# Performance work log

Measured on AMD Instinct MI355X. Metric: run time of the kernel, lower is better.

The kernel has to match this reference:

```python
import jax, jax.numpy as jnp
import numpy as np

NUM_ITERATIONS = 3

def _squash(s):
    # Original squash reduces over the trailing singleton dim -> elementwise.
    sn = s * s
    return sn * s / ((1.0 + sn) * jnp.sqrt(sn))

def setup_inputs() -> dict:
    key = jax.random.key(0)
    k1, k2 = jax.random.split(key)
    x = jax.random.normal(k1, (128, 1152, 8), dtype=jnp.float32)
    W = jax.random.normal(k2, (1, 1152, 16, 16, 8), dtype=jnp.float32)
    return {"x": x, "W": W}

def reference(x, W):
    # x: [B, R, I]; W: [1, R, C, O, I]
    Wr = W[0]  # [R, C, O, I]
    # u_hat = W @ x broadcast over capsules: [B, R, C, O]
    u_hat = jnp.einsum('rcoi,bri->brco', Wr, x)
    R, C = Wr.shape[0], Wr.shape[1]
    b = jnp.zeros((R, C), dtype=x.dtype)  # routing logits (shared across batch)
    v = None
    for it in range(NUM_ITERATIONS):
        # legacy F.softmax on [1,R,C,1] -> dim=1 == routes axis
        c = jax.nn.softmax(b, axis=0)  # [R, C]
        s = jnp.einsum('rc,brco->bco', c, u_hat)  # [B, C, O]
        v = _squash(s)
        if it < NUM_ITERATIONS - 1:
            # agreement: <u_hat, v> averaged over batch
            a = jnp.einsum('brco,bco->brc', u_hat, v).mean(axis=0)  # [R, C]
            b = b + a
    return v  # [B, C, O] == v_j.squeeze(1).squeeze(-1)
```

## Files before the change

### kernel.cpp

```cpp
#include <hip/hip_runtime.h>
#include <math.h>

#define B_   128
#define R_   1152
#define RS_  64
#define RCH_ 18
#define NBINS 72

#define WS_SP   0
#define WS_V    2097152
#define WS_BLOG 2129920
#define WS_CTRL 2148352
#define WS_WT   2150912

__device__ __forceinline__ float squashf(float s) {
    return s * fabsf(s) / (1.0f + s * s);
}

__global__ __launch_bounds__(512) void wtrans_k(const float* __restrict__ W,
                                                float* __restrict__ wt,
                                                float* __restrict__ ctrl) {
    const int r = blockIdx.x;
    const int t = threadIdx.x;
    __shared__ float4 sh[520];
    const float4* __restrict__ W4 = (const float4*)W;
    float4* __restrict__ Wt4 = (float4*)wt;

    if (r == 0) {
        for (int u = t; u < 2560; u += 512) ctrl[u] = 0.0f;
    }

    sh[(t & 7) * 65 + (t >> 3)] = W4[r * 512 + t];
    __syncthreads();
    Wt4[r * 512 + t] = sh[(t >> 6) * 65 + (t & 63)];
}

template <bool FIRST>
__global__ __launch_bounds__(256) void gemm_s_k(const float* __restrict__ x,
                                                const float* __restrict__ wt,
                                                const float* __restrict__ blog,
                                                const float* __restrict__ colbins,
                                                float* __restrict__ sp) {
    const int bt  = blockIdx.x;
    const int rs  = blockIdx.y;
    const int t   = threadIdx.x;
    const int co4 = t & 63;
    const int b4  = t >> 6;
    const int c   = co4 >> 2;
    const int r0  = rs * RCH_;

    __shared__ float4 xl4[288];
    __shared__ float  cwl[RCH_ * 16];
    __shared__ float  colinv_sh[16];
    __shared__ float  psum[256];

    const float4* __restrict__ X4  = (const float4*)x;
    const float4* __restrict__ Wt4 = (const float4*)wt;

    #pragma unroll
    for (int k = 0; k < 2; ++k) {
        const int u = t + k * 256;
        if (u < 288) {
            const int bl = u / 36, rem = u % 36;
            xl4[u] = X4[((bt * 8 + bl) * R_ + r0) * 2 + rem];
        }
    }

    if (!FIRST) {
        const int cc = t & 15, jb = t >> 4;
        float s = 0.f;
        for (int j = jb; j < NBINS; j += 16) s += colbins[j * 16 + cc];
        psum[t] = s;
        __syncthreads();
        if (t < 16) {
            float tot = 0.f;
            #pragma unroll
            for (int k2 = 0; k2 < 16; ++k2) tot += psum[k2 * 16 + t];
            colinv_sh[t] = 1.0f / tot;
        }
        __syncthreads();
        for (int u2 = t; u2 < RCH_ * 16; u2 += 256) {
            const int rl = u2 >> 4, c2 = u2 & 15;
            cwl[u2] = __expf(blog[(r0 + rl) * 16 + c2]) * colinv_sh[c2];
        }
    }
    __syncthreads();

    float acc[2][4];
    #pragma unroll
    for (int j = 0; j < 2; ++j)
        #pragma unroll
        for (int q = 0; q < 4; ++q) acc[j][q] = 0.f;

    #pragma unroll 3
    for (int rr = 0; rr < RCH_; ++rr) {
        const float cwv = FIRST ? (1.0f / (float)R_) : cwl[rr * 16 + c];
        const float4* wp = Wt4 + ((size_t)(r0 + rr) << 9) + co4;
        const float4 w0 = wp[  0], w1 = wp[ 64], w2 = wp[128], w3 = wp[192];
        const float4 w4 = wp[256], w5 = wp[320], w6 = wp[384], w7 = wp[448];
        #pragma unroll
        for (int j = 0; j < 2; ++j) {
            const float4 xa = xl4[(b4 * 2 + j) * 36 + rr * 2];
            const float4 xb = xl4[(b4 * 2 + j) * 36 + rr * 2 + 1];
            const float d0 = w0.x*xa.x + w0.y*xa.y + w0.z*xa.z + w0.w*xa.w
                           + w1.x*xb.x + w1.y*xb.y + w1.z*xb.z + w1.w*xb.w;
            const float d1 = w2.x*xa.x + w2.y*xa.y + w2.z*xa.z + w2.w*xa.w
                           + w3.x*xb.x + w3.y*xb.y + w3.z*xb.z + w3.w*xb.w;
            const float d2 = w4.x*xa.x + w4.y*xa.y + w4.z*xa.z + w4.w*xa.w
                           + w5.x*xb.x + w5.y*xb.y + w5.z*xb.z + w5.w*xb.w;
            const float d3 = w6.x*xa.x + w6.y*xa.y + w6.z*xa.z + w6.w*xa.w
                           + w7.x*xb.x + w7.y*xb.y + w7.z*xb.z + w7.w*xb.w;
            acc[j][0] = fmaf(cwv, d0, acc[j][0]);
            acc[j][1] = fmaf(cwv, d1, acc[j][1]);
            acc[j][2] = fmaf(cwv, d2, acc[j][2]);
            acc[j][3] = fmaf(cwv, d3, acc[j][3]);
        }
    }

    float4* sp4 = (float4*)sp;
    #pragma unroll
    for (int j = 0; j < 2; ++j) {
        const int b = bt * 8 + b4 * 2 + j;
        float4 o4; o4.x = acc[j][0]; o4.y = acc[j][1]; o4.z = acc[j][2]; o4.w = acc[j][3];
        sp4[(rs * B_ + b) * 64 + co4] = o4;
    }
}

__global__ __launch_bounds__(512) void reduce_squash_k(const float* __restrict__ sp,
                                                       float* __restrict__ outv) {
    const int t   = threadIdx.x;
    const int li  = t & 127;
    const int kq  = t >> 7;
    const int idx = blockIdx.x * 128 + li;
    const float* p = sp + (size_t)kq * 16 * 32768 + idx;
    float a0 = 0.f, a1 = 0.f, a2 = 0.f, a3 = 0.f;
    #pragma unroll
    for (int k = 0; k < 16; k += 4) {
        a0 += p[(k + 0) * 32768];
        a1 += p[(k + 1) * 32768];
        a2 += p[(k + 2) * 32768];
        a3 += p[(k + 3) * 32768];
    }
    __shared__ float red[512];
    red[t] = (a0 + a1) + (a2 + a3);
    __syncthreads();
    if (t < 128) {
        const float s = (red[t] + red[t + 128]) + (red[t + 256] + red[t + 384]);
        outv[idx] = squashf(s);
    }
}

template <bool FIRST>
__global__ __launch_bounds__(256, 2) void a_k(const float* __restrict__ x,
                                              const float* __restrict__ wt,
                                              const float* __restrict__ v,
                                              float* __restrict__ blog,
                                              float* __restrict__ colbins) {
    const int r = blockIdx.x;
    const int t = threadIdx.x;
    const int w = t >> 6, lane = t & 63;
    const int co4 = lane, c = lane >> 2;

    __shared__ float4 xl[256];
    __shared__ float  red[64];
    const float4* __restrict__ X4  = (const float4*)x;
    const float4* __restrict__ V4  = (const float4*)v;
    const float4* __restrict__ Wt4 = (const float4*)wt;

    xl[t] = X4[((t >> 1) * R_ + r) * 2 + (t & 1)];
    __syncthreads();

    float y[8][4];
    #pragma unroll
    for (int i = 0; i < 8; ++i)
        #pragma unroll
        for (int q = 0; q < 4; ++q) y[i][q] = 0.f;

    const int b0 = w * 32;
    #pragma unroll 4
    for (int bb = 0; bb < 32; ++bb) {
        const int b = b0 + bb;
        const float4 xa = xl[b * 2];
        const float4 xb = xl[b * 2 + 1];
        const float4 vv = V4[b * 64 + co4];
        y[0][0] = fmaf(xa.x, vv.x, y[0][0]); y[0][1] = fmaf(xa.x, vv.y, y[0][1]);
        y[0][2] = fmaf(xa.x, vv.z, y[0][2]); y[0][3] = fmaf(xa.x, vv.w, y[0][3]);
        y[1][0] = fmaf(xa.y, vv.x, y[1][0]); y[1][1] = fmaf(xa.y, vv.y, y[1][1]);
        y[1][2] = fmaf(xa.y, vv.z, y[1][2]); y[1][3] = fmaf(xa.y, vv.w, y[1][3]);
        y[2][0] = fmaf(xa.z, vv.x, y[2][0]); y[2][1] = fmaf(xa.z, vv.y, y[2][1]);
        y[2][2] = fmaf(xa.z, vv.z, y[2][2]); y[2][3] = fmaf(xa.z, vv.w, y[2][3]);
        y[3][0] = fmaf(xa.w, vv.x, y[3][0]); y[3][1] = fmaf(xa.w, vv.y, y[3][1]);
        y[3][2] = fmaf(xa.w, vv.z, y[3][2]); y[3][3] = fmaf(xa.w, vv.w, y[3][3]);
        y[4][0] = fmaf(xb.x, vv.x, y[4][0]); y[4][1] = fmaf(xb.x, vv.y, y[4][1]);
        y[4][2] = fmaf(xb.x, vv.z, y[4][2]); y[4][3] = fmaf(xb.x, vv.w, y[4][3]);
        y[5][0] = fmaf(xb.y, vv.x, y[5][0]); y[5][1] = fmaf(xb.y, vv.y, y[5][1]);
        y[5][2] = fmaf(xb.y, vv.z, y[5][2]); y[5][3] = fmaf(xb.y, vv.w, y[5][3]);
        y[6][0] = fmaf(xb.z, vv.x, y[6][0]); y[6][1] = fmaf(xb.z, vv.y, y[6][1]);
        y[6][2] = fmaf(xb.z, vv.z, y[6][2]); y[6][3] = fmaf(xb.z, vv.w, y[6][3]);
        y[7][0] = fmaf(xb.w, vv.x, y[7][0]); y[7][1] = fmaf(xb.w, vv.y, y[7][1]);
        y[7][2] = fmaf(xb.w, vv.z, y[7][2]); y[7][3] = fmaf(xb.w, vv.w, y[7][3]);
    }

    const float4* wp = Wt4 + ((size_t)r << 9) + co4;
    float part = 0.f;
    #pragma unroll
    for (int q = 0; q < 4; ++q) {
        const float4 w0 = wp[(2 * q) * 64];
        const float4 w1 = wp[(2 * q + 1) * 64];
        part += w0.x*y[0][q] + w0.y*y[1][q] + w0.z*y[2][q] + w0.w*y[3][q]
              + w1.x*y[4][q] + w1.y*y[5][q] + w1.z*y[6][q] + w1.w*y[7][q];
    }
    part += __shfl_xor(part, 1);
    part += __shfl_xor(part, 2);
    if ((lane & 3) == 0) red[w * 16 + c] = part;
    __syncthreads();
    if (t < 16) {
        const float val = ((red[t] + red[16 + t]) + (red[32 + t] + red[48 + t]))
                          * (1.0f / (float)B_);
        const int idx = r * 16 + t;
        const float nv = FIRST ? val : (blog[idx] + val);
        blog[idx] = nv;
        atomicAdd(&colbins[(r >> 4) * 16 + t], __expf(nv));
    }
}

extern "C" void kernel_launch(void* const* d_in, const int* in_sizes, int n_in,
                              void* d_out, int out_size, void* d_ws, size_t ws_size,
                              hipStream_t stream) {
    const float* x = (const float*)d_in[0];
    const float* W = (const float*)d_in[1];
    float* out = (float*)d_out;
    float* ws  = (float*)d_ws;

    float* sp   = ws + WS_SP;
    float* v    = ws + WS_V;
    float* blog = ws + WS_BLOG;
    float* ctrl = ws + WS_CTRL;
    float* wt   = ws + WS_WT;

    float* cs0 = ctrl;
    float* cs1 = ctrl + 1280;

    wtrans_k<<<R_, 512, 0, stream>>>(W, wt, ctrl);

    gemm_s_k<true ><<<dim3(16, RS_), 256, 0, stream>>>(x, wt, nullptr, nullptr, sp);
    reduce_squash_k<<<256, 512, 0, stream>>>(sp, v);
    a_k<true ><<<R_, 256, 0, stream>>>(x, wt, v, blog, cs0);

    gemm_s_k<false><<<dim3(16, RS_), 256, 0, stream>>>(x, wt, blog, cs0, sp);
    reduce_squash_k<<<256, 512, 0, stream>>>(sp, v);
    a_k<false><<<R_, 256, 0, stream>>>(x, wt, v, blog, cs1);

    gemm_s_k<false><<<dim3(16, RS_), 256, 0, stream>>>(x, wt, blog, cs1, sp);
    reduce_squash_k<<<256, 512, 0, stream>>>(sp, out);
}
```

Measured before the change: 168.0 us.

## Fuse split-R reduction and squash into gemm via atomics and last-block finalize

Each gemm block now atomically accumulates its partial s into a small [B,C,O] buffer instead of writing per-slice partials. The last block to finish, found with a global counter, applies squash, writes v, and clears s, so the separate reduce kernels and the 8 MB partial buffer go away. It also pre-transposes x into a per-route layout in the first kernel so a_k reads it contiguously. In exchange it adds float atomic contention, a serialized tail where a single block squashes 32K elements, and summation order that varies between runs.

```diff
diff --git a/kernel.cpp b/kernel.cpp
--- a/kernel.cpp
+++ b/kernel.cpp
@@ -6,28 +6,39 @@
 #define RS_  64
 #define RCH_ 18
 #define NBINS 72
-
-#define WS_SP   0
-#define WS_V    2097152
-#define WS_BLOG 2129920
-#define WS_CTRL 2148352
-#define WS_WT   2150912
+#define NBLK_G 1024
+
+#define WS_S    0
+#define WS_V    32768
+#define WS_BLOG 65536
+#define WS_CTRL 84480
+#define WS_XT   86912
+#define WS_WT   1266560
 
 __device__ __forceinline__ float squashf(float s) {
     return s * fabsf(s) / (1.0f + s * s);
 }
 
 __global__ __launch_bounds__(512) void wtrans_k(const float* __restrict__ W,
+                                                const float* __restrict__ x,
                                                 float* __restrict__ wt,
+                                                float* __restrict__ xt,
+                                                float* __restrict__ s,
                                                 float* __restrict__ ctrl) {
     const int r = blockIdx.x;
     const int t = threadIdx.x;
     __shared__ float4 sh[520];
     const float4* __restrict__ W4 = (const float4*)W;
+    const float4* __restrict__ X4 = (const float4*)x;
     float4* __restrict__ Wt4 = (float4*)wt;
-
+    float4* __restrict__ XT4 = (float4*)xt;
+
+    if (r < 64) s[r * 512 + t] = 0.0f;
     if (r == 0) {
-        for (int u = t; u < 2560; u += 512) ctrl[u] = 0.0f;
+        for (int u = t; u < 2368; u += 512) ctrl[u] = 0.0f;
+    }
+    if (t < 256) {
+        XT4[r * 256 + t] = X4[((t >> 1) * R_ + r) * 2 + (t & 1)];
     }
 
     sh[(t & 7) * 65 + (t >> 3)] = W4[r * 512 + t];
@@ -35,12 +46,14 @@
     Wt4[r * 512 + t] = sh[(t >> 6) * 65 + (t & 63)];
 }
 
-template <bool FIRST>
+template <int IT>
 __global__ __launch_bounds__(256) void gemm_s_k(const float* __restrict__ x,
                                                 const float* __restrict__ wt,
                                                 const float* __restrict__ blog,
                                                 const float* __restrict__ colbins,
-                                                float* __restrict__ sp) {
+                                                float* __restrict__ s,
+                                                float* __restrict__ dst,
+                                                unsigned int* __restrict__ ctr) {
     const int bt  = blockIdx.x;
     const int rs  = blockIdx.y;
     const int t   = threadIdx.x;
@@ -53,6 +66,7 @@
     __shared__ float  cwl[RCH_ * 16];
     __shared__ float  colinv_sh[16];
     __shared__ float  psum[256];
+    __shared__ unsigned int old_sh;
 
     const float4* __restrict__ X4  = (const float4*)x;
     const float4* __restrict__ Wt4 = (const float4*)wt;
@@ -66,11 +80,11 @@
         }
     }
 
-    if (!FIRST) {
+    if (IT != 0) {
         const int cc = t & 15, jb = t >> 4;
-        float s = 0.f;
-        for (int j = jb; j < NBINS; j += 16) s += colbins[j * 16 + cc];
-        psum[t] = s;
+        float sm = 0.f;
+        for (int j = jb; j < NBINS; j += 16) sm += colbins[j * 16 + cc];
+        psum[t] = sm;
         __syncthreads();
         if (t < 16) {
             float tot = 0.f;
@@ -94,7 +108,7 @@
 
     #pragma unroll 3
     for (int rr = 0; rr < RCH_; ++rr) {
-        const float cwv = FIRST ? (1.0f / (float)R_) : cwl[rr * 16 + c];
+        const float cwv = (IT == 0) ? (1.0f / (float)R_) : cwl[rr * 16 + c];
         const float4* wp = Wt4 + ((size_t)(r0 + rr) << 9) + co4;
         const float4 w0 = wp[  0], w1 = wp[ 64], w2 = wp[128], w3 = wp[192];
         const float4 w4 = wp[256], w5 = wp[320], w6 = wp[384], w7 = wp[448];
@@ -117,41 +131,36 @@
         }
     }
 
-    float4* sp4 = (float4*)sp;
     #pragma unroll
     for (int j = 0; j < 2; ++j) {
         const int b = bt * 8 + b4 * 2 + j;
-        float4 o4; o4.x = acc[j][0]; o4.y = acc[j][1]; o4.z = acc[j][2]; o4.w = acc[j][3];
-        sp4[(rs * B_ + b) * 64 + co4] = o4;
-    }
-}
-
-__global__ __launch_bounds__(512) void reduce_squash_k(const float* __restrict__ sp,
-                                                       float* __restrict__ outv) {
-    const int t   = threadIdx.x;
-    const int li  = t & 127;
-    const int kq  = t >> 7;
-    const int idx = blockIdx.x * 128 + li;
-    const float* p = sp + (size_t)kq * 16 * 32768 + idx;
-    float a0 = 0.f, a1 = 0.f, a2 = 0.f, a3 = 0.f;
-    #pragma unroll
-    for (int k = 0; k < 16; k += 4) {
-        a0 += p[(k + 0) * 32768];
-        a1 += p[(k + 1) * 32768];
-        a2 += p[(k + 2) * 32768];
-        a3 += p[(k + 3) * 32768];
-    }
-    __shared__ float red[512];
-    red[t] = (a0 + a1) + (a2 + a3);
-    __syncthreads();
-    if (t < 128) {
-        const float s = (red[t] + red[t + 128]) + (red[t + 256] + red[t + 384]);
-        outv[idx] = squashf(s);
+        float* sb = s + b * 256 + co4 * 4;
+        atomicAdd(&sb[0], acc[j][0]);
+        atomicAdd(&sb[1], acc[j][1]);
+        atomicAdd(&sb[2], acc[j][2]);
+        atomicAdd(&sb[3], acc[j][3]);
+    }
+
+    __syncthreads();
+    if (t == 0) {
+        __threadfence();
+        old_sh = atomicAdd(ctr, 1u);
+    }
+    __syncthreads();
+    if (old_sh != (unsigned int)(NBLK_G - 1)) return;
+
+    #pragma unroll 8
+    for (int k = 0; k < 128; ++k) {
+        const int u = t + k * 256;
+        const float sv = __hip_atomic_load(&s[u], __ATOMIC_RELAXED,
+                                           __HIP_MEMORY_SCOPE_AGENT);
+        dst[u] = squashf(sv);
+        if (IT < 2) s[u] = 0.0f;
     }
 }
 
 template <bool FIRST>
-__global__ __launch_bounds__(256, 2) void a_k(const float* __restrict__ x,
+__global__ __launch_bounds__(256, 2) void a_k(const float* __restrict__ xt,
                                               const float* __restrict__ wt,
                                               const float* __restrict__ v,
                                               float* __restrict__ blog,
@@ -163,11 +172,11 @@
 
     __shared__ float4 xl[256];
     __shared__ float  red[64];
-    const float4* __restrict__ X4  = (const float4*)x;
+    const float4* __restrict__ XT4 = (const float4*)xt;
     const float4* __restrict__ V4  = (const float4*)v;
     const float4* __restrict__ Wt4 = (const float4*)wt;
 
-    xl[t] = X4[((t >> 1) * R_ + r) * 2 + (t & 1)];
+    xl[t] = XT4[r * 256 + t];
     __syncthreads();
 
     float y[8][4];
@@ -232,25 +241,24 @@
     float* out = (float*)d_out;
     float* ws  = (float*)d_ws;
 
-    float* sp   = ws + WS_SP;
+    float* s    = ws + WS_S;
     float* v    = ws + WS_V;
     float* blog = ws + WS_BLOG;
     float* ctrl = ws + WS_CTRL;
+    float* xt   = ws + WS_XT;
     float* wt   = ws + WS_WT;
 
-    float* cs0 = ctrl;
-    float* cs1 = ctrl + 1280;
-
-    wtrans_k<<<R_, 512, 0, stream>>>(W, wt, ctrl);
-
-    gemm_s_k<true ><<<dim3(16, RS_), 256, 0, stream>>>(x, wt, nullptr, nullptr, sp);
-    reduce_squash_k<<<256, 512, 0, stream>>>(sp, v);
-    a_k<true ><<<R_, 256, 0, stream>>>(x, wt, v, blog, cs0);
-
-    gemm_s_k<false><<<dim3(16, RS_), 256, 0, stream>>>(x, wt, blog, cs0, sp);
-    reduce_squash_k<<<256, 512, 0, stream>>>(sp, v);
-    a_k<false><<<R_, 256, 0, stream>>>(x, wt, v, blog, cs1);
-
-    gemm_s_k<false><<<dim3(16, RS_), 256, 0, stream>>>(x, wt, blog, cs1, sp);
-    reduce_squash_k<<<256, 512, 0, stream>>>(sp, out);
-}
+    unsigned int* ctr = (unsigned int*)ctrl;
+    float* cs0 = ctrl + 64;
+    float* cs1 = ctrl + 1216;
+
+    wtrans_k<<<R_, 512, 0, stream>>>(W, x, wt, xt, s, ctrl);
+
+    gemm_s_k<0><<<dim3(16, RS_), 256, 0, stream>>>(x, wt, nullptr, nullptr, s, v, ctr + 0);
+    a_k<true ><<<R_, 256, 0, stream>>>(xt, wt, v, blog, cs0);
+
+    gemm_s_k<1><<<dim3(16, RS_), 256, 0, stream>>>(x, wt, blog, cs0, s, v, ctr + 16);
+    a_k<false><<<R_, 256, 0, stream>>>(xt, wt, v, blog, cs1);
+
+    gemm_s_k<2><<<dim3(16, RS_), 256, 0, stream>>>(x, wt, blog, cs1, s, out, ctr + 32);
+}
```

New measurement: 395.9 us. 136% more time.

## Fuse W transpose into first GEMM, pre-transpose x, process two routes per a_k block

Applied to the files above, without the earlier changes.

Drops the standalone W transpose kernel. The first s-GEMM now reads W in its original layout, and blocks with bt==0 write the transposed copy for later iterations, so one launch and one full pass over W go away. That GEMM also writes a route-major transposed copy of x and zeroes the control buffers. a_k now handles two routes per block using the transposed x, which halves the grid and reuses each v load for two routes, at the cost of more registers per thread.

```diff
diff --git a/kernel.cpp b/kernel.cpp
--- a/kernel.cpp
+++ b/kernel.cpp
@@ -11,36 +11,22 @@
 #define WS_V    2097152
 #define WS_BLOG 2129920
 #define WS_CTRL 2148352
-#define WS_WT   2150912
+#define WS_XT   2150784
+#define WS_WT   3330432
 
 __device__ __forceinline__ float squashf(float s) {
     return s * fabsf(s) / (1.0f + s * s);
 }
 
-__global__ __launch_bounds__(512) void wtrans_k(const float* __restrict__ W,
+template <int IT>
+__global__ __launch_bounds__(256) void gemm_s_k(const float* __restrict__ x,
+                                                const float* __restrict__ W,
                                                 float* __restrict__ wt,
-                                                float* __restrict__ ctrl) {
-    const int r = blockIdx.x;
-    const int t = threadIdx.x;
-    __shared__ float4 sh[520];
-    const float4* __restrict__ W4 = (const float4*)W;
-    float4* __restrict__ Wt4 = (float4*)wt;
-
-    if (r == 0) {
-        for (int u = t; u < 2560; u += 512) ctrl[u] = 0.0f;
-    }
-
-    sh[(t & 7) * 65 + (t >> 3)] = W4[r * 512 + t];
-    __syncthreads();
-    Wt4[r * 512 + t] = sh[(t >> 6) * 65 + (t & 63)];
-}
-
-template <bool FIRST>
-__global__ __launch_bounds__(256) void gemm_s_k(const float* __restrict__ x,
-                                                const float* __restrict__ wt,
+                                                float* __restrict__ xt,
                                                 const float* __restrict__ blog,
                                                 const float* __restrict__ colbins,
-                                                float* __restrict__ sp) {
+                                                float* __restrict__ sp,
+                                                float* __restrict__ ctrl) {
     const int bt  = blockIdx.x;
     const int rs  = blockIdx.y;
     const int t   = threadIdx.x;
@@ -55,7 +41,9 @@
     __shared__ float  psum[256];
 
     const float4* __restrict__ X4  = (const float4*)x;
-    const float4* __restrict__ Wt4 = (const float4*)wt;
+    const float4* __restrict__ W4  = (const float4*)W;
+    float4* __restrict__ Wt4 = (float4*)wt;
+    float4* __restrict__ XT4 = (float4*)xt;
 
     #pragma unroll
     for (int k = 0; k < 2; ++k) {
@@ -66,11 +54,21 @@
         }
     }
 
-    if (!FIRST) {
+    if (IT == 0) {
+        if (bt == 1) {
+            for (int rr = 0; rr < RCH_; ++rr) {
+                const int r = r0 + rr;
+                XT4[r * 256 + t] = X4[((t >> 1) * R_ + r) * 2 + (t & 1)];
+            }
+        }
+        if (bt == 2 && rs == 0) {
+            for (int u = t; u < 2432; u += 256) ctrl[u] = 0.0f;
+        }
+    } else {
         const int cc = t & 15, jb = t >> 4;
-        float s = 0.f;
-        for (int j = jb; j < NBINS; j += 16) s += colbins[j * 16 + cc];
-        psum[t] = s;
+        float sm = 0.f;
+        for (int j = jb; j < NBINS; j += 16) sm += colbins[j * 16 + cc];
+        psum[t] = sm;
         __syncthreads();
         if (t < 16) {
             float tot = 0.f;
@@ -94,10 +92,22 @@
 
     #pragma unroll 3
     for (int rr = 0; rr < RCH_; ++rr) {
-        const float cwv = FIRST ? (1.0f / (float)R_) : cwl[rr * 16 + c];
-        const float4* wp = Wt4 + ((size_t)(r0 + rr) << 9) + co4;
-        const float4 w0 = wp[  0], w1 = wp[ 64], w2 = wp[128], w3 = wp[192];
-        const float4 w4 = wp[256], w5 = wp[320], w6 = wp[384], w7 = wp[448];
+        const float cwv = (IT == 0) ? (1.0f / (float)R_) : cwl[rr * 16 + c];
+        float4 w0, w1, w2, w3, w4, w5, w6, w7;
+        if (IT == 0) {
+            const float4* wp = W4 + ((size_t)(r0 + rr) << 9) + co4 * 8;
+            w0 = wp[0]; w1 = wp[1]; w2 = wp[2]; w3 = wp[3];
+            w4 = wp[4]; w5 = wp[5]; w6 = wp[6]; w7 = wp[7];
+            if (bt == 0) {
+                float4* wo = Wt4 + ((size_t)(r0 + rr) << 9) + co4;
+                wo[  0] = w0; wo[ 64] = w1; wo[128] = w2; wo[192] = w3;
+                wo[256] = w4; wo[320] = w5; wo[384] = w6; wo[448] = w7;
+            }
+        } else {
+            const float4* wp = Wt4 + ((size_t)(r0 + rr) << 9) + co4;
+            w0 = wp[  0]; w1 = wp[ 64]; w2 = wp[128]; w3 = wp[192];
+            w4 = wp[256]; w5 = wp[320]; w6 = wp[384]; w7 = wp[448];
+        }
         #pragma unroll
         for (int j = 0; j < 2; ++j) {
             const float4 xa = xl4[(b4 * 2 + j) * 36 + rr * 2];
@@ -150,77 +160,98 @@
     }
 }
 
+#define ACC32(Y, XA, XB) \
+    Y[0][0]=fmaf(XA.x,vv.x,Y[0][0]); Y[0][1]=fmaf(XA.x,vv.y,Y[0][1]); \
+    Y[0][2]=fmaf(XA.x,vv.z,Y[0][2]); Y[0][3]=fmaf(XA.x,vv.w,Y[0][3]); \
+    Y[1][0]=fmaf(XA.y,vv.x,Y[1][0]); Y[1][1]=fmaf(XA.y,vv.y,Y[1][1]); \
+    Y[1][2]=fmaf(XA.y,vv.z,Y[1][2]); Y[1][3]=fmaf(XA.y,vv.w,Y[1][3]); \
+    Y[2][0]=fmaf(XA.z,vv.x,Y[2][0]); Y[2][1]=fmaf(XA.z,vv.y,Y[2][1]); \
+    Y[2][2]=fmaf(XA.z,vv.z,Y[2][2]); Y[2][3]=fmaf(XA.z,vv.w,Y[2][3]); \
+    Y[3][0]=fmaf(XA.w,vv.x,Y[3][0]); Y[3][1]=fmaf(XA.w,vv.y,Y[3][1]); \
+    Y[3][2]=fmaf(XA.w,vv.z,Y[3][2]); Y[3][3]=fmaf(XA.w,vv.w,Y[3][3]); \
+    Y[4][0]=fmaf(XB.x,vv.x,Y[4][0]); Y[4][1]=fmaf(XB.x,vv.y,Y[4][1]); \
+    Y[4][2]=fmaf(XB.x,vv.z,Y[4][2]); Y[4][3]=fmaf(XB.x,vv.w,Y[4][3]); \
+    Y[5][0]=fmaf(XB.y,vv.x,Y[5][0]); Y[5][1]=fmaf(XB.y,vv.y,Y[5][1]); \
+    Y[5][2]=fmaf(XB.y,vv.z,Y[5][2]); Y[5][3]=fmaf(XB.y,vv.w,Y[5][3]); \
+    Y[6][0]=fmaf(XB.z,vv.x,Y[6][0]); Y[6][1]=fmaf(XB.z,vv.y,Y[6][1]); \
+    Y[6][2]=fmaf(XB.z,vv.z,Y[6][2]); Y[6][3]=fmaf(XB.z,vv.w,Y[6][3]); \
+    Y[7][0]=fmaf(XB.w,vv.x,Y[7][0]); Y[7][1]=fmaf(XB.w,vv.y,Y[7][1]); \
+    Y[7][2]=fmaf(XB.w,vv.z,Y[7][2]); Y[7][3]=fmaf(XB.w,vv.w,Y[7][3]);
+
 template <bool FIRST>
-__global__ __launch_bounds__(256, 2) void a_k(const float* __restrict__ x,
+__global__ __launch_bounds__(256, 2) void a_k(const float* __restrict__ xt,
                                               const float* __restrict__ wt,
                                               const float* __restrict__ v,
                                               float* __restrict__ blog,
                                               float* __restrict__ colbins) {
-    const int r = blockIdx.x;
-    const int t = threadIdx.x;
-    const int w = t >> 6, lane = t & 63;
+    const int r0 = blockIdx.x * 2;
+    const int t  = threadIdx.x;
+    const int w  = t >> 6, lane = t & 63;
     const int co4 = lane, c = lane >> 2;
 
-    __shared__ float4 xl[256];
-    __shared__ float  red[64];
-    const float4* __restrict__ X4  = (const float4*)x;
+    __shared__ float4 xl[512];
+    __shared__ float  red[128];
+    const float4* __restrict__ XT4 = (const float4*)xt;
     const float4* __restrict__ V4  = (const float4*)v;
     const float4* __restrict__ Wt4 = (const float4*)wt;
 
-    xl[t] = X4[((t >> 1) * R_ + r) * 2 + (t & 1)];
-    __syncthreads();
-
-    float y[8][4];
+    #pragma unroll
+    for (int k = 0; k < 2; ++k) {
+        const int u = t + k * 256;
+        xl[u] = XT4[(r0 + ((u & 3) >> 1)) * 256 + (u >> 2) * 2 + (u & 1)];
+    }
+    __syncthreads();
+
+    float y0[8][4], y1[8][4];
     #pragma unroll
     for (int i = 0; i < 8; ++i)
         #pragma unroll
-        for (int q = 0; q < 4; ++q) y[i][q] = 0.f;
+        for (int q = 0; q < 4; ++q) { y0[i][q] = 0.f; y1[i][q] = 0.f; }
 
     const int b0 = w * 32;
-    #pragma unroll 4
+    #pragma unroll 2
     for (int bb = 0; bb < 32; ++bb) {
         const int b = b0 + bb;
-        const float4 xa = xl[b * 2];
-        const float4 xb = xl[b * 2 + 1];
-        const float4 vv = V4[b * 64 + co4];
-        y[0][0] = fmaf(xa.x, vv.x, y[0][0]); y[0][1] = fmaf(xa.x, vv.y, y[0][1]);
-        y[0][2] = fmaf(xa.x, vv.z, y[0][2]); y[0][3] = fmaf(xa.x, vv.w, y[0][3]);
-        y[1][0] = fmaf(xa.y, vv.x, y[1][0]); y[1][1] = fmaf(xa.y, vv.y, y[1][1]);
-        y[1][2] = fmaf(xa.y, vv.z, y[1][2]); y[1][3] = fmaf(xa.y, vv.w, y[1][3]);
-        y[2][0] = fmaf(xa.z, vv.x, y[2][0]); y[2][1] = fmaf(xa.z, vv.y, y[2][1]);
-        y[2][2] = fmaf(xa.z, vv.z, y[2][2]); y[2][3] = fmaf(xa.z, vv.w, y[2][3]);
-        y[3][0] = fmaf(xa.w, vv.x, y[3][0]); y[3][1] = fmaf(xa.w, vv.y, y[3][1]);
-        y[3][2] = fmaf(xa.w, vv.z, y[3][2]); y[3][3] = fmaf(xa.w, vv.w, y[3][3]);
-        y[4][0] = fmaf(xb.x, vv.x, y[4][0]); y[4][1] = fmaf(xb.x, vv.y, y[4][1]);
-        y[4][2] = fmaf(xb.x, vv.z, y[4][2]); y[4][3] = fmaf(xb.x, vv.w, y[4][3]);
-        y[5][0] = fmaf(xb.y, vv.x, y[5][0]); y[5][1] = fmaf(xb.y, vv.y, y[5][1]);
-        y[5][2] = fmaf(xb.y, vv.z, y[5][2]); y[5][3] = fmaf(xb.y, vv.w, y[5][3]);
-        y[6][0] = fmaf(xb.z, vv.x, y[6][0]); y[6][1] = fmaf(xb.z, vv.y, y[6][1]);
-        y[6][2] = fmaf(xb.z, vv.z, y[6][2]); y[6][3] = fmaf(xb.z, vv.w, y[6][3]);
-        y[7][0] = fmaf(xb.w, vv.x, y[7][0]); y[7][1] = fmaf(xb.w, vv.y, y[7][1]);
-        y[7][2] = fmaf(xb.w, vv.z, y[7][2]); y[7][3] = fmaf(xb.w, vv.w, y[7][3]);
-    }
-
-    const float4* wp = Wt4 + ((size_t)r << 9) + co4;
-    float part = 0.f;
-    #pragma unroll
-    for (int q = 0; q < 4; ++q) {
-        const float4 w0 = wp[(2 * q) * 64];
-        const float4 w1 = wp[(2 * q + 1) * 64];
-        part += w0.x*y[0][q] + w0.y*y[1][q] + w0.z*y[2][q] + w0.w*y[3][q]
-              + w1.x*y[4][q] + w1.y*y[5][q] + w1.z*y[6][q] + w1.w*y[7][q];
-    }
-    part += __shfl_xor(part, 1);
-    part += __shfl_xor(part, 2);
-    if ((lane & 3) == 0) red[w * 16 + c] = part;
-    __syncthreads();
-    if (t < 16) {
-        const float val = ((red[t] + red[16 + t]) + (red[32 + t] + red[48 + t]))
+        const float4 xa0 = xl[b * 4 + 0];
+        const float4 xb0 = xl[b * 4 + 1];
+        const float4 xa1 = xl[b * 4 + 2];
+        const float4 xb1 = xl[b * 4 + 3];
+        const float4 vv  = V4[b * 64 + co4];
+        ACC32(y0, xa0, xb0)
+        ACC32(y1, xa1, xb1)
+    }
+
+    float part0 = 0.f, part1 = 0.f;
+    {
+        const float4* wp0 = Wt4 + ((size_t)r0 << 9) + co4;
+        const float4* wp1 = Wt4 + ((size_t)(r0 + 1) << 9) + co4;
+        #pragma unroll
+        for (int q = 0; q < 4; ++q) {
+            const float4 a0 = wp0[(2 * q) * 64], a1 = wp0[(2 * q + 1) * 64];
+            part0 += a0.x*y0[0][q] + a0.y*y0[1][q] + a0.z*y0[2][q] + a0.w*y0[3][q]
+                   + a1.x*y0[4][q] + a1.y*y0[5][q] + a1.z*y0[6][q] + a1.w*y0[7][q];
+            const float4 b0v = wp1[(2 * q) * 64], b1v = wp1[(2 * q + 1) * 64];
+            part1 += b0v.x*y1[0][q] + b0v.y*y1[1][q] + b0v.z*y1[2][q] + b0v.w*y1[3][q]
+                   + b1v.x*y1[4][q] + b1v.y*y1[5][q] + b1v.z*y1[6][q] + b1v.w*y1[7][q];
+        }
+    }
+    part0 += __shfl_xor(part0, 1); part0 += __shfl_xor(part0, 2);
+    part1 += __shfl_xor(part1, 1); part1 += __shfl_xor(part1, 2);
+    if ((lane & 3) == 0) {
+        red[w * 16 + c]      = part0;
+        red[64 + w * 16 + c] = part1;
+    }
+    __syncthreads();
+    if (t < 32) {
+        const int rr2 = t >> 4, cc = t & 15;
+        const float* rb = red + rr2 * 64;
+        const float val = ((rb[cc] + rb[16 + cc]) + (rb[32 + cc] + rb[48 + cc]))
                           * (1.0f / (float)B_);
-        const int idx = r * 16 + t;
+        const int r = r0 + rr2;
+        const int idx = r * 16 + cc;
         const float nv = FIRST ? val : (blog[idx] + val);
         blog[idx] = nv;
-        atomicAdd(&colbins[(r >> 4) * 16 + t], __expf(nv));
+        atomicAdd(&colbins[(r >> 4) * 16 + cc], __expf(nv));
     }
 }
 
@@ -236,21 +267,20 @@
     float* v    = ws + WS_V;
     float* blog = ws + WS_BLOG;
     float* ctrl = ws + WS_CTRL;
+    float* xt   = ws + WS_XT;
     float* wt   = ws + WS_WT;
 
     float* cs0 = ctrl;
     float* cs1 = ctrl + 1280;
 
-    wtrans_k<<<R_, 512, 0, stream>>>(W, wt, ctrl);
-
-    gemm_s_k<true ><<<dim3(16, RS_), 256, 0, stream>>>(x, wt, nullptr, nullptr, sp);
+    gemm_s_k<0><<<dim3(16, RS_), 256, 0, stream>>>(x, W, wt, xt, nullptr, nullptr, sp, ctrl);
     reduce_squash_k<<<256, 512, 0, stream>>>(sp, v);
-    a_k<true ><<<R_, 256, 0, stream>>>(x, wt, v, blog, cs0);
-
-    gemm_s_k<false><<<dim3(16, RS_), 256, 0, stream>>>(x, wt, blog, cs0, sp);
+    a_k<true ><<<576, 256, 0, stream>>>(xt, wt, v, blog, cs0);
+
+    gemm_s_k<1><<<dim3(16, RS_), 256, 0, stream>>>(x, W, wt, xt, blog, cs0, sp, ctrl);
     reduce_squash_k<<<256, 512, 0, stream>>>(sp, v);
-    a_k<false><<<R_, 256, 0, stream>>>(x, wt, v, blog, cs1);
-
-    gemm_s_k<false><<<dim3(16, RS_), 256, 0, stream>>>(x, wt, blog, cs1, sp);
+    a_k<false><<<576, 256, 0, stream>>>(xt, wt, v, blog, cs1);
+
+    gemm_s_k<2><<<dim3(16, RS_), 256, 0, stream>>>(x, W, wt, xt, blog, cs1, sp, ctrl);
     reduce_squash_k<<<256, 512, 0, stream>>>(sp, out);
 }
```

Result: slower. 229.1 us (+36.4%).

## Fuse W transpose into first gemm pass with double-buffered shared-memory staging

Applied to the files above, without the earlier changes.

Removes the standalone transpose kernel and has the first s-GEMM pass read W directly, transposing each route's slice through a double-buffered shared-memory tile with prefetch of the next route. Blocks with bt==0 write the transposed W to the workspace for later passes, and the control-buffer zeroing moves into one block of this kernel. This saves a launch and one full pass over W, but adds a __syncthreads per route step and a larger shared-memory footprint, which may lower occupancy. Some correctness risk also comes from other blocks zeroing ctrl concurrently and the shrunk workspace offset.

```diff
diff --git a/kernel.cpp b/kernel.cpp
--- a/kernel.cpp
+++ b/kernel.cpp
@@ -11,36 +11,20 @@
 #define WS_V    2097152
 #define WS_BLOG 2129920
 #define WS_CTRL 2148352
-#define WS_WT   2150912
+#define WS_WT   2150784
 
 __device__ __forceinline__ float squashf(float s) {
     return s * fabsf(s) / (1.0f + s * s);
 }
 
-__global__ __launch_bounds__(512) void wtrans_k(const float* __restrict__ W,
+template <int IT>
+__global__ __launch_bounds__(256) void gemm_s_k(const float* __restrict__ x,
+                                                const float* __restrict__ W,
                                                 float* __restrict__ wt,
-                                                float* __restrict__ ctrl) {
-    const int r = blockIdx.x;
-    const int t = threadIdx.x;
-    __shared__ float4 sh[520];
-    const float4* __restrict__ W4 = (const float4*)W;
-    float4* __restrict__ Wt4 = (float4*)wt;
-
-    if (r == 0) {
-        for (int u = t; u < 2560; u += 512) ctrl[u] = 0.0f;
-    }
-
-    sh[(t & 7) * 65 + (t >> 3)] = W4[r * 512 + t];
-    __syncthreads();
-    Wt4[r * 512 + t] = sh[(t >> 6) * 65 + (t & 63)];
-}
-
-template <bool FIRST>
-__global__ __launch_bounds__(256) void gemm_s_k(const float* __restrict__ x,
-                                                const float* __restrict__ wt,
                                                 const float* __restrict__ blog,
                                                 const float* __restrict__ colbins,
-                                                float* __restrict__ sp) {
+                                                float* __restrict__ sp,
+                                                float* __restrict__ ctrl) {
     const int bt  = blockIdx.x;
     const int rs  = blockIdx.y;
     const int t   = threadIdx.x;
@@ -50,12 +34,14 @@
     const int r0  = rs * RCH_;
 
     __shared__ float4 xl4[288];
+    __shared__ float4 wsh[2][520];
     __shared__ float  cwl[RCH_ * 16];
     __shared__ float  colinv_sh[16];
     __shared__ float  psum[256];
 
     const float4* __restrict__ X4  = (const float4*)x;
-    const float4* __restrict__ Wt4 = (const float4*)wt;
+    const float4* __restrict__ W4  = (const float4*)W;
+    float4* __restrict__ Wt4 = (float4*)wt;
 
     #pragma unroll
     for (int k = 0; k < 2; ++k) {
@@ -66,11 +52,19 @@
         }
     }
 
-    if (!FIRST) {
+    if (IT == 0) {
+        if (bt == 2 && rs == 0) {
+            for (int u = t; u < 2432; u += 256) ctrl[u] = 0.0f;
+        }
+        const float4* wrow = W4 + ((size_t)r0 << 9);
+        wsh[0][(t & 7) * 65 + (t >> 3)] = wrow[t];
+        const int u2 = t + 256;
+        wsh[0][(u2 & 7) * 65 + (u2 >> 3)] = wrow[u2];
+    } else {
         const int cc = t & 15, jb = t >> 4;
-        float s = 0.f;
-        for (int j = jb; j < NBINS; j += 16) s += colbins[j * 16 + cc];
-        psum[t] = s;
+        float sm = 0.f;
+        for (int j = jb; j < NBINS; j += 16) sm += colbins[j * 16 + cc];
+        psum[t] = sm;
         __syncthreads();
         if (t < 16) {
             float tot = 0.f;
@@ -94,10 +88,37 @@
 
     #pragma unroll 3
     for (int rr = 0; rr < RCH_; ++rr) {
-        const float cwv = FIRST ? (1.0f / (float)R_) : cwl[rr * 16 + c];
-        const float4* wp = Wt4 + ((size_t)(r0 + rr) << 9) + co4;
-        const float4 w0 = wp[  0], w1 = wp[ 64], w2 = wp[128], w3 = wp[192];
-        const float4 w4 = wp[256], w5 = wp[320], w6 = wp[384], w7 = wp[448];
+        const float cwv = (IT == 0) ? (1.0f / (float)R_) : cwl[rr * 16 + c];
+        float4 w0, w1, w2, w3, w4, w5, w6, w7;
+        if (IT == 0) {
+            const int p = rr & 1;
+            float4 pf0, pf1;
+            const bool pf = (rr < RCH_ - 1);
+            if (pf) {
+                const float4* wrow = W4 + ((size_t)(r0 + rr + 1) << 9);
+                pf0 = wrow[t];
+                pf1 = wrow[t + 256];
+            }
+            w0 = wsh[p][0 * 65 + co4]; w1 = wsh[p][1 * 65 + co4];
+            w2 = wsh[p][2 * 65 + co4]; w3 = wsh[p][3 * 65 + co4];
+            w4 = wsh[p][4 * 65 + co4]; w5 = wsh[p][5 * 65 + co4];
+            w6 = wsh[p][6 * 65 + co4]; w7 = wsh[p][7 * 65 + co4];
+            if (bt == 0) {
+                float4* wo = Wt4 + ((size_t)(r0 + rr) << 9) + co4;
+                wo[  0] = w0; wo[ 64] = w1; wo[128] = w2; wo[192] = w3;
+                wo[256] = w4; wo[320] = w5; wo[384] = w6; wo[448] = w7;
+            }
+            if (pf) {
+                wsh[p ^ 1][(t & 7) * 65 + (t >> 3)] = pf0;
+                const int u2 = t + 256;
+                wsh[p ^ 1][(u2 & 7) * 65 + (u2 >> 3)] = pf1;
+                __syncthreads();
+            }
+        } else {
+            const float4* wp = Wt4 + ((size_t)(r0 + rr) << 9) + co4;
+            w0 = wp[  0]; w1 = wp[ 64]; w2 = wp[128]; w3 = wp[192];
+            w4 = wp[256]; w5 = wp[320]; w6 = wp[384]; w7 = wp[448];
+        }
         #pragma unroll
         for (int j = 0; j < 2; ++j) {
             const float4 xa = xl4[(b4 * 2 + j) * 36 + rr * 2];
@@ -241,16 +262,14 @@
     float* cs0 = ctrl;
     float* cs1 = ctrl + 1280;
 
-    wtrans_k<<<R_, 512, 0, stream>>>(W, wt, ctrl);
-
-    gemm_s_k<true ><<<dim3(16, RS_), 256, 0, stream>>>(x, wt, nullptr, nullptr, sp);
+    gemm_s_k<0><<<dim3(16, RS_), 256, 0, stream>>>(x, W, wt, nullptr, nullptr, sp, ctrl);
     reduce_squash_k<<<256, 512, 0, stream>>>(sp, v);
     a_k<true ><<<R_, 256, 0, stream>>>(x, wt, v, blog, cs0);
 
-    gemm_s_k<false><<<dim3(16, RS_), 256, 0, stream>>>(x, wt, blog, cs0, sp);
+    gemm_s_k<1><<<dim3(16, RS_), 256, 0, stream>>>(x, W, wt, blog, cs0, sp, ctrl);
     reduce_squash_k<<<256, 512, 0, stream>>>(sp, v);
     a_k<false><<<R_, 256, 0, stream>>>(x, wt, v, blog, cs1);
 
-    gemm_s_k<false><<<dim3(16, RS_), 256, 0, stream>>>(x, wt, blog, cs1, sp);
+    gemm_s_k<1><<<dim3(16, RS_), 256, 0, stream>>>(x, W, wt, blog, cs1, sp, ctrl);
     reduce_squash_k<<<256, 512, 0, stream>>>(sp, out);
 }
```

Measured after the change: 181.0 us. +7.8%, slower.
